# Kernel optimization log

Hardware: AMD Instinct MI355X
Metric: run time of the kernel (lower is better)

Reference implementation:

```python
import jax, jax.numpy as jnp
import numpy as np

KS = 3
STRIDE = 1
PAD = 1


def conv2d(x, w, b=None, stride=1, pad=0):
    out = jax.lax.conv_general_dilated(
        x, w, (stride, stride), [(pad, pad), (pad, pad)],
        dimension_numbers=('NCHW', 'OIHW', 'NCHW'))
    if b is not None:
        out = out + b[None, :, None, None]
    return out


def _get_p(offset, ks, stride):
    # offset: (b, 2N, h, w); returns sampling coords p = p_0 + p_n + offset
    b, c2, h, w = offset.shape
    N = c2 // 2
    r = (ks - 1) // 2
    pn_x, pn_y = jnp.meshgrid(jnp.arange(-r, r + 1), jnp.arange(-r, r + 1), indexing='ij')
    p_n = jnp.concatenate([pn_x.reshape(-1), pn_y.reshape(-1)]).astype(offset.dtype)  # (2N,)
    p0_x, p0_y = jnp.meshgrid(jnp.arange(1, h * stride + 1, stride),
                              jnp.arange(1, w * stride + 1, stride), indexing='ij')
    p0 = jnp.concatenate([jnp.broadcast_to(p0_x, (N, h, w)),
                          jnp.broadcast_to(p0_y, (N, h, w))], 0).astype(offset.dtype)  # (2N,h,w)
    return offset + p_n[None, :, None, None] + p0[None]


def _gather_hw(src, qx, qy):
    # src: (b,c,H,W); qx,qy: (b,h,w,N) int -> (b,c,h,w,N)
    b, c, H, W = src.shape
    flat = src.reshape(b, c, H * W)
    idx = (qx * W + qy).reshape(b, -1)
    out = jax.vmap(lambda f, i: f[:, i])(flat, idx)  # (b,c,h*w*N)
    return out.reshape(b, c, qx.shape[1], qx.shape[2], qx.shape[3])


def _bilinear(src_pad, p, Hc, Wc, N):
    # p: (b,h,w,2N); clamp bounds (Hc,Wc) follow the torch code (may differ from src_pad dims)
    px, py = p[..., :N], p[..., N:]
    fx, fy = jnp.floor(px), jnp.floor(py)
    qlt_x = jnp.clip(fx, 0, Hc - 1).astype(jnp.int32)
    qlt_y = jnp.clip(fy, 0, Wc - 1).astype(jnp.int32)
    qrb_x = jnp.clip(fx + 1, 0, Hc - 1).astype(jnp.int32)
    qrb_y = jnp.clip(fy + 1, 0, Wc - 1).astype(jnp.int32)
    pxc = jnp.clip(px, 0, Hc - 1)
    pyc = jnp.clip(py, 0, Wc - 1)
    g_lt = (1 + (qlt_x - pxc)) * (1 + (qlt_y - pyc))
    g_rb = (1 - (qrb_x - pxc)) * (1 - (qrb_y - pyc))
    g_lb = (1 + (qlt_x - pxc)) * (1 - (qrb_y - pyc))
    g_rt = (1 - (qrb_x - pxc)) * (1 + (qlt_y - pyc))
    v_lt = _gather_hw(src_pad, qlt_x, qlt_y)
    v_rb = _gather_hw(src_pad, qrb_x, qrb_y)
    v_lb = _gather_hw(src_pad, qlt_x, qrb_y)
    v_rt = _gather_hw(src_pad, qrb_x, qlt_y)
    return (g_lt[:, None] * v_lt + g_rb[:, None] * v_rb
            + g_lb[:, None] * v_lb + g_rt[:, None] * v_rt)


def setup_inputs() -> dict:
    key = jax.random.key(0)
    k1, k2, k3, k4 = jax.random.split(key, 4)
    B, C, H, W = 2, 64, 128, 128
    OUTC, KSZ = 64, KS
    N = KSZ * KSZ
    x = jax.random.normal(k1, (B, C, H, W), dtype=jnp.float32)
    depth = jax.random.uniform(k2, (B, 1, H, W), dtype=jnp.float32)
    w_p = jax.random.normal(k3, (2 * N, C, 3, 3), dtype=jnp.float32) * 0.01
    b_p = jnp.zeros((2 * N,), dtype=jnp.float32)
    w_conv = jax.random.normal(k4, (OUTC, C, KSZ, KSZ), dtype=jnp.float32) * 0.05
    return {'x': x, 'depth': depth, 'w_p': w_p, 'b_p': b_p, 'w_conv': w_conv}


def reference(x, depth, w_p, b_p, w_conv):
    ks, stride, pad = KS, STRIDE, PAD
    N = ks * ks
    b, c, H, W = x.shape
    offset = conv2d(x, w_p, b_p, stride=stride, pad=1)  # (b, 2N, h, w)
    depth_pad = jnp.pad(depth, ((0, 0), (0, 0), (pad, pad), (pad, pad)))
    # pass 1: sample depth; torch clamps against UNPADDED x dims here (quirk preserved)
    p = jnp.transpose(_get_p(offset, ks, stride), (0, 2, 3, 1))  # (b,h,w,2N)
    depth_offset = _bilinear(depth_pad, p, H, W, N)  # (b,1,h,w,N)
    depth_diff = jnp.abs(depth[..., None] - depth_offset)  # (b,1,h,w,N)
    depth_weight = jnp.exp(-4.0 * depth_diff) + 0.25
    dw = jnp.concatenate([depth_weight, depth_weight], axis=-1)  # (b,1,h,w,2N)
    dw = jnp.transpose(dw, (0, 4, 2, 3, 1))[..., 0]  # (b,2N,h,w)
    offset = offset * dw
    # pass 2: sample x from padded x, clamped to padded dims
    x_pad = jnp.pad(x, ((0, 0), (0, 0), (pad, pad), (pad, pad)))
    Hp, Wp = x_pad.shape[2], x_pad.shape[3]
    p = jnp.transpose(_get_p(offset, ks, stride), (0, 2, 3, 1))
    x_offset = _bilinear(x_pad, p, Hp, Wp, N)  # (b,c,h,w,N)
    m = jnp.exp(-1.0 * depth_diff)  # (b,1,h,w,N), broadcasts over c
    x_offset = x_offset * m
    # reshape (b,c,h,w,N) -> (b,c,h*ks,w*ks) matching _reshape_x_offset
    b2, c2, h, w, _ = x_offset.shape
    xo = x_offset.reshape(b2, c2, h, w, ks, ks)
    xo = jnp.transpose(xo, (0, 1, 2, 4, 3, 5)).reshape(b2, c2, h * ks, w * ks)
    out = conv2d(xo, w_conv, None, stride=ks, pad=0)  # (b,outc,h,w)
    return out
```

## Files before the change

kernel.cpp:

```cpp
#include <hip/hip_runtime.h>
#include <math.h>


typedef __attribute__((ext_vector_type(8))) short bf16x8;
typedef __attribute__((ext_vector_type(4))) short s16x4;
typedef __attribute__((ext_vector_type(4))) float f32x4;

#define MFMA16(a, b, c) __builtin_amdgcn_mfma_f32_16x16x32_bf16((a), (b), (c), 0, 0, 0)

__device__ __forceinline__ float bf2f(short v) {
    return __uint_as_float(((unsigned)(unsigned short)v) << 16);
}
__device__ __forceinline__ short f2bf(float f) {
    unsigned u = __float_as_uint(f);
    u = u + 0x7fffu + ((u >> 16) & 1u);
    return (short)(u >> 16);
}

__global__ __launch_bounds__(256) void k_prep(const float* __restrict__ x,
                                              const float* __restrict__ w_conv,
                                              const float* __restrict__ w_p,
                                              short* __restrict__ xT,
                                              short* __restrict__ xTlo,
                                              short* __restrict__ wK,
                                              short* __restrict__ wPh,
                                              short* __restrict__ wPl) {
    __shared__ short sH[128][72];
    __shared__ short sL[128][72];
    int bid = blockIdx.x;
    int tid = threadIdx.x;
    if (bid < 256) {
        int p = tid & 127;
        int halfc = tid >> 7;
        int pix0 = bid << 7;
        int b = pix0 >> 14;
        const float* xb = x + (size_t)b * 64 * 16384 + (pix0 & 16383);
#pragma unroll
        for (int cc = 0; cc < 8; ++cc) {
            int c0 = cc * 8 + halfc * 4;
            union { short s[4]; s16x4 v; } hi, lo;
#pragma unroll
            for (int e = 0; e < 4; ++e) {
                float v = xb[(c0 + e) * 16384 + p];
                short hb = f2bf(v);
                hi.s[e] = hb;
                lo.s[e] = f2bf(v - bf2f(hb));
            }
            *reinterpret_cast<s16x4*>(&sH[p][c0]) = hi.v;
            *reinterpret_cast<s16x4*>(&sL[p][c0]) = lo.v;
        }
        __syncthreads();
        short* xTo = xT   + ((size_t)pix0 << 6);
        short* xLo = xTlo + ((size_t)pix0 << 6);
#pragma unroll
        for (int r = 0; r < 4; ++r) {
            int u = (r << 8) + tid;
            int pp = u >> 3, ch8 = u & 7;
            *reinterpret_cast<bf16x8*>(xTo + pp * 64 + ch8 * 8) =
                *reinterpret_cast<const bf16x8*>(&sH[pp][ch8 * 8]);
            *reinterpret_cast<bf16x8*>(xLo + pp * 64 + ch8 * 8) =
                *reinterpret_cast<const bf16x8*>(&sL[pp][ch8 * 8]);
        }
    } else {
        int idx = (bid - 256) * 256 + tid;
        if (idx >= 55296) return;
        if (idx < 36864) {
            int e = idx & 7, o = (idx >> 3) & 63, h = (idx >> 9) & 3, s = idx >> 11;
            int k = s * 32 + h * 8 + e;
            int n = k >> 6, c = k & 63;
            wK[idx] = f2bf(w_conv[o * 576 + c * 9 + n]);
        } else {
            int j = idx - 36864;
            int e = j & 7, m = (j >> 3) & 31, h = (j >> 8) & 3, s = j >> 10;
            int k = s * 32 + h * 8 + e;
            int t = k >> 6, c = k & 63;
            float v = (m < 18) ? w_p[m * 576 + c * 9 + t] : 0.f;
            short hb = f2bf(v);
            wPh[j] = hb;
            wPl[j] = f2bf(v - bf2f(hb));
        }
    }
}

__global__ __launch_bounds__(256, 4) void k_fused(const short* __restrict__ xT,
                                                  const short* __restrict__ xTlo,
                                                  const short* __restrict__ wPh,
                                                  const short* __restrict__ wPl,
                                                  const short* __restrict__ wK,
                                                  const float* __restrict__ depth,
                                                  const float* __restrict__ b_p,
                                                  float* __restrict__ out) {
    __shared__ __align__(16) char smem[24880];
    short* win    = (short*)smem;
    float* part1  = (float*)(smem + 13440);
    float* dwin   = (float*)(smem + 18560);
    float* offs   = (float*)(smem + 18992);
    float* pmw    = (float*)(smem + 20272);
    float* accred = (float*)smem;
    float* obuf   = (float*)(smem + 13440);

    int tid = threadIdx.x;
    int lane = tid & 63;
    int wv = tid >> 6;
    int l15 = lane & 15, h = lane >> 4;
    int bid = blockIdx.x;
    int swz = (bid & 7) * 256 + (bid >> 3);
    int pb = swz << 4;
    int b = pb >> 14, i = (pb & 16383) >> 7, j0 = pb & 127;
    const short* xTb  = xT   + ((size_t)b << 20);
    const short* xTlb = xTlo + ((size_t)b << 20);
    const float* db = depth + (b << 14);

    for (int u = tid; u < 840; u += 256) {
        int c8 = u & 7, px = u >> 3;
        int wr = px / 21, wc = px % 21;
        int r = i - 2 + wr, c = j0 - 2 + wc;
        bf16x8 v = {0, 0, 0, 0, 0, 0, 0, 0};
        if ((unsigned)r < 128u && (unsigned)c < 128u)
            v = *reinterpret_cast<const bf16x8*>(xTb + ((size_t)(r * 128 + c) << 6) + c8 * 8);
        *reinterpret_cast<bf16x8*>((char*)win + px * 128 + ((c8 ^ (px & 7)) << 4)) = v;
    }
    if (tid < 105) {
        int wr = tid / 21, wc = tid % 21;
        int r = i - 2 + wr, c = j0 - 2 + wc;
        dwin[tid] = ((unsigned)r < 128u && (unsigned)c < 128u) ? db[r * 128 + c] : 0.f;
    }
    __syncthreads();

    f32x4 acc0 = {0.f, 0.f, 0.f, 0.f}, acc1 = {0.f, 0.f, 0.f, 0.f};
    for (int t = wv; t < 9; t += 4) {
        int wp = (t / 3 + 1) * 21 + (l15 + t % 3 + 1);
        int si = i + t / 3 - 1;
        int sj = j0 + l15 + t % 3 - 1;
        bool inb = ((unsigned)si < 128u && (unsigned)sj < 128u);
        size_t go = (size_t)(si * 128 + sj) << 6;
#pragma unroll
        for (int par = 0; par < 2; ++par) {
            int s_ = t * 2 + par;
            int c8 = par * 4 + h;
            bf16x8 bh = *reinterpret_cast<const bf16x8*>(
                (char*)win + wp * 128 + ((c8 ^ (wp & 7)) << 4));
            bf16x8 bl = {0, 0, 0, 0, 0, 0, 0, 0};
            if (inb) bl = *reinterpret_cast<const bf16x8*>(xTlb + go + c8 * 8);
            const short* wh_ = wPh + (size_t)((s_ * 4 + h) * 32 + l15) * 8;
            const short* wl_ = wPl + (size_t)((s_ * 4 + h) * 32 + l15) * 8;
            bf16x8 ah0 = *reinterpret_cast<const bf16x8*>(wh_);
            bf16x8 ah1 = *reinterpret_cast<const bf16x8*>(wh_ + 128);
            bf16x8 al0 = *reinterpret_cast<const bf16x8*>(wl_);
            bf16x8 al1 = *reinterpret_cast<const bf16x8*>(wl_ + 128);
            acc0 = MFMA16(ah0, bh, acc0);
            acc1 = MFMA16(ah1, bh, acc1);
            acc0 = MFMA16(ah0, bl, acc0);
            acc1 = MFMA16(ah1, bl, acc1);
            acc0 = MFMA16(al0, bh, acc0);
            acc1 = MFMA16(al1, bh, acc1);
        }
    }
#pragma unroll
    for (int r = 0; r < 4; ++r) {
        part1[wv * 320 + l15 * 20 + h * 4 + r] = acc0[r];
        int o1 = 16 + h * 4 + r;
        if (o1 < 18) part1[wv * 320 + l15 * 20 + o1] = acc1[r];
    }
    __syncthreads();
    if (tid < 128) {
        for (int u = tid; u < 288; u += 128) {
            int p = u / 18, o = u % 18;
            offs[p * 20 + o] = part1[p * 20 + o] + part1[320 + p * 20 + o] +
                               part1[640 + p * 20 + o] + part1[960 + p * 20 + o] + b_p[o];
        }
    }
    __syncthreads();

    int g = (wv << 2) + h;
    if (g < 9) {
        int n = g;
        float offx = offs[l15 * 20 + n];
        float offy = offs[l15 * 20 + 9 + n];
        float gx = (float)(n / 3 - 1 + i + 1);
        float gy = (float)(n % 3 - 1 + j0 + l15 + 1);
        float dctr = dwin[2 * 21 + l15 + 2];
        float p1x = offx + gx, p1y = offy + gy;
        float fx = floorf(p1x), fy = floorf(p1y);
        float qltx = fminf(fmaxf(fx, 0.f), 127.f);
        float qlty = fminf(fmaxf(fy, 0.f), 127.f);
        float qrbx = fminf(fmaxf(fx + 1.f, 0.f), 127.f);
        float qrby = fminf(fmaxf(fy + 1.f, 0.f), 127.f);
        float pxc = fminf(fmaxf(p1x, 0.f), 127.f);
        float pyc = fminf(fmaxf(p1y, 0.f), 127.f);
        float glt = (1.f + (qltx - pxc)) * (1.f + (qlty - pyc));
        float grb = (1.f - (qrbx - pxc)) * (1.f - (qrby - pyc));
        float glb = (1.f + (qltx - pxc)) * (1.f - (qrby - pyc));
        float grt = (1.f - (qrbx - pxc)) * (1.f + (qlty - pyc));
        int ilx = (int)qltx, ily = (int)qlty, irx = (int)qrbx, iry = (int)qrby;
        auto dv = [&](int qx, int qy) -> float {
            if (qx < 1 || qx > 128 || qy < 1 || qy > 128) return 0.f;
            int r = qx - 1, c = qy - 1;
            int wr = r - (i - 2), wc = c - (j0 - 2);
            if ((unsigned)wr < 5u && (unsigned)wc < 21u) return dwin[wr * 21 + wc];
            return db[r * 128 + c];
        };
        float dof = glt * dv(ilx, ily) + grb * dv(irx, iry) + glb * dv(ilx, iry) + grt * dv(irx, ily);
        float dd = fabsf(dctr - dof);
        float dwn = expf(-4.f * dd) + 0.25f;
        float mn = expf(-dd);
        float px = offx * dwn + gx;
        float py = offy * dwn + gy;
        float fx2 = floorf(px), fy2 = floorf(py);
        float xltx = fminf(fmaxf(fx2, 0.f), 129.f);
        float xlty = fminf(fmaxf(fy2, 0.f), 129.f);
        float xrbx = fminf(fmaxf(fx2 + 1.f, 0.f), 129.f);
        float xrby = fminf(fmaxf(fy2 + 1.f, 0.f), 129.f);
        float xpxc = fminf(fmaxf(px, 0.f), 129.f);
        float xpyc = fminf(fmaxf(py, 0.f), 129.f);
        float wlt = (1.f + (xltx - xpxc)) * (1.f + (xlty - xpyc));
        float wrb = (1.f - (xrbx - xpxc)) * (1.f - (xrby - xpyc));
        float wlb = (1.f + (xltx - xpxc)) * (1.f - (xrby - xpyc));
        float wrt = (1.f - (xrbx - xpxc)) * (1.f + (xlty - xpyc));
        int jlx = (int)xltx, jly = (int)xlty, jrx = (int)xrbx, jry = (int)xrby;
        float* d = pmw + (l15 * 9 + n) * 8;
        int* di = (int*)(d + 4);
        auto mk = [&](int qx, int qy, float gw, int slot) {
            bool ok = (qx >= 1 && qx <= 128 && qy >= 1 && qy <= 128);
            d[slot] = ok ? gw * mn : 0.f;
            int idx = 0;
            if (ok) {
                int r = qx - 1, c = qy - 1;
                int wr = r - (i - 2), wc = c - (j0 - 2);
                idx = ((unsigned)wr < 5u && (unsigned)wc < 21u) ? (wr * 21 + wc)
                                                                : (-1 - (r * 128 + c));
            }
            di[slot] = idx;
        };
        mk(jlx, jly, wlt, 0);
        mk(jrx, jry, wrb, 1);
        mk(jlx, jry, wlb, 2);
        mk(jrx, jly, wrt, 3);
    }
    __syncthreads();

    f32x4 A0 = {0.f, 0.f, 0.f, 0.f}, A1 = {0.f, 0.f, 0.f, 0.f};
    f32x4 A2 = {0.f, 0.f, 0.f, 0.f}, A3 = {0.f, 0.f, 0.f, 0.f};
    for (int n = wv; n < 9; n += 4) {
        const float* ww = pmw + (l15 * 9 + n) * 8;
        float4 w4 = *reinterpret_cast<const float4*>(ww);
        int4 i4 = *reinterpret_cast<const int4*>(ww + 4);
        const short* wk0 = wK + (size_t)((n * 8 + h) * 64 + l15) * 8;
        const short* wk1 = wk0 + 2048;
        bf16x8 a00 = *reinterpret_cast<const bf16x8*>(wk0);
        bf16x8 a01 = *reinterpret_cast<const bf16x8*>(wk0 + 128);
        bf16x8 a02 = *reinterpret_cast<const bf16x8*>(wk0 + 256);
        bf16x8 a03 = *reinterpret_cast<const bf16x8*>(wk0 + 384);
        bf16x8 a10 = *reinterpret_cast<const bf16x8*>(wk1);
        bf16x8 a11 = *reinterpret_cast<const bf16x8*>(wk1 + 128);
        bf16x8 a12 = *reinterpret_cast<const bf16x8*>(wk1 + 256);
        bf16x8 a13 = *reinterpret_cast<const bf16x8*>(wk1 + 384);
        const int* ip = &i4.x;
        const float* wp = &w4.x;
#pragma unroll
        for (int t = 0; t < 4; ++t) {
            int idx = ip[t];
            float w = wp[t];
            bf16x8 th0, th1;
            if (idx >= 0) {
                const char* base = (char*)win + idx * 128;
                th0 = *reinterpret_cast<const bf16x8*>(base + ((h ^ (idx & 7)) << 4));
                th1 = *reinterpret_cast<const bf16x8*>(base + (((4 + h) ^ (idx & 7)) << 4));
            } else {
                int gp = -1 - idx;
                const short* gb = xTb + ((size_t)gp << 6) + h * 8;
                th0 = *reinterpret_cast<const bf16x8*>(gb);
                th1 = *reinterpret_cast<const bf16x8*>(gb + 32);
            }
            f32x4 Z = {0.f, 0.f, 0.f, 0.f};
            f32x4 D0 = MFMA16(a00, th0, Z);
            f32x4 D1 = MFMA16(a01, th0, Z);
            f32x4 D2 = MFMA16(a02, th0, Z);
            f32x4 D3 = MFMA16(a03, th0, Z);
            D0 = MFMA16(a10, th1, D0);
            D1 = MFMA16(a11, th1, D1);
            D2 = MFMA16(a12, th1, D2);
            D3 = MFMA16(a13, th1, D3);
            A0 += w * D0;
            A1 += w * D1;
            A2 += w * D2;
            A3 += w * D3;
        }
    }
    __syncthreads();
    if (wv != 0) {
        float* ar = accred + (wv - 1) * 1024 + lane * 16;
        *reinterpret_cast<f32x4*>(ar)      = A0;
        *reinterpret_cast<f32x4*>(ar + 4)  = A1;
        *reinterpret_cast<f32x4*>(ar + 8)  = A2;
        *reinterpret_cast<f32x4*>(ar + 12) = A3;
    }
    __syncthreads();
    if (wv == 0) {
        const float* a1 = accred + lane * 16;
        const float* a2 = accred + 1024 + lane * 16;
        const float* a3 = accred + 2048 + lane * 16;
#pragma unroll
        for (int r = 0; r < 4; ++r) {
            obuf[(h * 4 + r) * 17 + l15]      = A0[r] + a1[r] + a2[r] + a3[r];
            obuf[(16 + h * 4 + r) * 17 + l15] = A1[r] + a1[4 + r] + a2[4 + r] + a3[4 + r];
            obuf[(32 + h * 4 + r) * 17 + l15] = A2[r] + a1[8 + r] + a2[8 + r] + a3[8 + r];
            obuf[(48 + h * 4 + r) * 17 + l15] = A3[r] + a1[12 + r] + a2[12 + r] + a3[12 + r];
        }
    }
    __syncthreads();
#pragma unroll
    for (int r = 0; r < 4; ++r) {
        int u = (r << 8) + tid;
        int o = u >> 4, p = u & 15;
        out[((size_t)(b * 64 + o) << 14) + (i << 7) + j0 + p] = obuf[o * 17 + p];
    }
}

extern "C" void kernel_launch(void* const* d_in, const int* in_sizes, int n_in,
                              void* d_out, int out_size, void* d_ws, size_t ws_size,
                              hipStream_t stream) {
    (void)in_sizes; (void)n_in; (void)out_size; (void)ws_size;
    const float* x      = (const float*)d_in[0];
    const float* depth  = (const float*)d_in[1];
    const float* w_p    = (const float*)d_in[2];
    const float* b_p    = (const float*)d_in[3];
    const float* w_conv = (const float*)d_in[4];
    float* out = (float*)d_out;

    char* wsb = (char*)d_ws;
    short* xT   = (short*)wsb;
    short* xTlo = (short*)(wsb + 4194304);
    short* wK   = (short*)(wsb + 8388608);
    short* wPh  = (short*)(wsb + 8462336);
    short* wPl  = (short*)(wsb + 8499200);

    hipLaunchKernelGGL(k_prep,  dim3(472),  dim3(256), 0, stream,
                       x, w_conv, w_p, xT, xTlo, wK, wPh, wPl);
    hipLaunchKernelGGL(k_fused, dim3(2048), dim3(256), 0, stream,
                       xT, xTlo, wPh, wPl, wK, depth, b_p, out);
}
```

Before: 42.41 us.

## Enlarge fused block tile to 64 pixels with 512 threads

Each block of the fused deformable-conv kernel now covers 64 pixels of a row instead of 16, using 512 threads (8 waves). Waves are split into 4 pixel groups times 2 channel halves, replacing the previous 4-way split over kernel taps. The larger shared input window (5x69 instead of 5x21) lowers the halo overhead and the number of redundant window loads per pixel. In exchange, LDS per block grows to about 79 KB and there are 512 blocks instead of 2048, which lowers occupancy and gives fewer blocks per CU.

```diff
diff --git a/kernel.cpp b/kernel.cpp
--- a/kernel.cpp
+++ b/kernel.cpp
@@ -82,7 +82,7 @@
     }
 }
 
-__global__ __launch_bounds__(256, 4) void k_fused(const short* __restrict__ xT,
+__global__ __launch_bounds__(512, 4) void k_fused(const short* __restrict__ xT,
                                                   const short* __restrict__ xTlo,
                                                   const short* __restrict__ wPh,
                                                   const short* __restrict__ wPl,
@@ -90,96 +90,98 @@
                                                   const float* __restrict__ depth,
                                                   const float* __restrict__ b_p,
                                                   float* __restrict__ out) {
-    __shared__ __align__(16) char smem[24880];
+    __shared__ __align__(16) char smem[79360];
     short* win    = (short*)smem;
-    float* part1  = (float*)(smem + 13440);
-    float* dwin   = (float*)(smem + 18560);
-    float* offs   = (float*)(smem + 18992);
-    float* pmw    = (float*)(smem + 20272);
+    float* dwin   = (float*)(smem + 44160);
+    float* part1  = (float*)(smem + 45568);
+    float* offs   = (float*)(smem + 55808);
+    float* pmw    = (float*)(smem + 60928);
     float* accred = (float*)smem;
-    float* obuf   = (float*)(smem + 13440);
+    float* obuf   = (float*)(smem + 16384);
 
     int tid = threadIdx.x;
     int lane = tid & 63;
     int wv = tid >> 6;
     int l15 = lane & 15, h = lane >> 4;
+    int ps = wv & 3;
+    int kh = wv >> 2;
+    int p0 = ps << 4;
     int bid = blockIdx.x;
-    int swz = (bid & 7) * 256 + (bid >> 3);
-    int pb = swz << 4;
+    int swz = (bid & 7) * 64 + (bid >> 3);
+    int pb = swz << 6;
     int b = pb >> 14, i = (pb & 16383) >> 7, j0 = pb & 127;
     const short* xTb  = xT   + ((size_t)b << 20);
     const short* xTlb = xTlo + ((size_t)b << 20);
     const float* db = depth + (b << 14);
 
-    for (int u = tid; u < 840; u += 256) {
+    for (int u = tid; u < 2760; u += 512) {
         int c8 = u & 7, px = u >> 3;
-        int wr = px / 21, wc = px % 21;
+        int wr = px / 69, wc = px % 69;
         int r = i - 2 + wr, c = j0 - 2 + wc;
         bf16x8 v = {0, 0, 0, 0, 0, 0, 0, 0};
         if ((unsigned)r < 128u && (unsigned)c < 128u)
             v = *reinterpret_cast<const bf16x8*>(xTb + ((size_t)(r * 128 + c) << 6) + c8 * 8);
         *reinterpret_cast<bf16x8*>((char*)win + px * 128 + ((c8 ^ (px & 7)) << 4)) = v;
     }
-    if (tid < 105) {
-        int wr = tid / 21, wc = tid % 21;
+    for (int u = tid; u < 345; u += 512) {
+        int wr = u / 69, wc = u % 69;
         int r = i - 2 + wr, c = j0 - 2 + wc;
-        dwin[tid] = ((unsigned)r < 128u && (unsigned)c < 128u) ? db[r * 128 + c] : 0.f;
+        dwin[u] = ((unsigned)r < 128u && (unsigned)c < 128u) ? db[r * 128 + c] : 0.f;
     }
     __syncthreads();
 
     f32x4 acc0 = {0.f, 0.f, 0.f, 0.f}, acc1 = {0.f, 0.f, 0.f, 0.f};
-    for (int t = wv; t < 9; t += 4) {
-        int wp = (t / 3 + 1) * 21 + (l15 + t % 3 + 1);
+    int c8p = kh * 4 + h;
+#pragma unroll
+    for (int t = 0; t < 9; ++t) {
+        int s_ = t * 2 + kh;
+        int wp = (t / 3 + 1) * 69 + (p0 + l15 + t % 3 + 1);
+        bf16x8 bh = *reinterpret_cast<const bf16x8*>(
+            (char*)win + wp * 128 + ((c8p ^ (wp & 7)) << 4));
         int si = i + t / 3 - 1;
-        int sj = j0 + l15 + t % 3 - 1;
-        bool inb = ((unsigned)si < 128u && (unsigned)sj < 128u);
-        size_t go = (size_t)(si * 128 + sj) << 6;
-#pragma unroll
-        for (int par = 0; par < 2; ++par) {
-            int s_ = t * 2 + par;
-            int c8 = par * 4 + h;
-            bf16x8 bh = *reinterpret_cast<const bf16x8*>(
-                (char*)win + wp * 128 + ((c8 ^ (wp & 7)) << 4));
-            bf16x8 bl = {0, 0, 0, 0, 0, 0, 0, 0};
-            if (inb) bl = *reinterpret_cast<const bf16x8*>(xTlb + go + c8 * 8);
-            const short* wh_ = wPh + (size_t)((s_ * 4 + h) * 32 + l15) * 8;
-            const short* wl_ = wPl + (size_t)((s_ * 4 + h) * 32 + l15) * 8;
-            bf16x8 ah0 = *reinterpret_cast<const bf16x8*>(wh_);
-            bf16x8 ah1 = *reinterpret_cast<const bf16x8*>(wh_ + 128);
-            bf16x8 al0 = *reinterpret_cast<const bf16x8*>(wl_);
-            bf16x8 al1 = *reinterpret_cast<const bf16x8*>(wl_ + 128);
-            acc0 = MFMA16(ah0, bh, acc0);
-            acc1 = MFMA16(ah1, bh, acc1);
-            acc0 = MFMA16(ah0, bl, acc0);
-            acc1 = MFMA16(ah1, bl, acc1);
-            acc0 = MFMA16(al0, bh, acc0);
-            acc1 = MFMA16(al1, bh, acc1);
-        }
-    }
-#pragma unroll
-    for (int r = 0; r < 4; ++r) {
-        part1[wv * 320 + l15 * 20 + h * 4 + r] = acc0[r];
-        int o1 = 16 + h * 4 + r;
-        if (o1 < 18) part1[wv * 320 + l15 * 20 + o1] = acc1[r];
-    }
-    __syncthreads();
-    if (tid < 128) {
-        for (int u = tid; u < 288; u += 128) {
-            int p = u / 18, o = u % 18;
-            offs[p * 20 + o] = part1[p * 20 + o] + part1[320 + p * 20 + o] +
-                               part1[640 + p * 20 + o] + part1[960 + p * 20 + o] + b_p[o];
-        }
-    }
-    __syncthreads();
-
-    int g = (wv << 2) + h;
-    if (g < 9) {
-        int n = g;
-        float offx = offs[l15 * 20 + n];
-        float offy = offs[l15 * 20 + 9 + n];
+        int sj = j0 + p0 + l15 + t % 3 - 1;
+        bf16x8 bl = {0, 0, 0, 0, 0, 0, 0, 0};
+        if ((unsigned)si < 128u && (unsigned)sj < 128u)
+            bl = *reinterpret_cast<const bf16x8*>(
+                xTlb + ((size_t)(si * 128 + sj) << 6) + c8p * 8);
+        const short* wh_ = wPh + (size_t)((s_ * 4 + h) * 32 + l15) * 8;
+        const short* wl_ = wPl + (size_t)((s_ * 4 + h) * 32 + l15) * 8;
+        bf16x8 ah0 = *reinterpret_cast<const bf16x8*>(wh_);
+        bf16x8 ah1 = *reinterpret_cast<const bf16x8*>(wh_ + 128);
+        bf16x8 al0 = *reinterpret_cast<const bf16x8*>(wl_);
+        bf16x8 al1 = *reinterpret_cast<const bf16x8*>(wl_ + 128);
+        acc0 = MFMA16(ah0, bh, acc0);
+        acc1 = MFMA16(ah1, bh, acc1);
+        acc0 = MFMA16(ah0, bl, acc0);
+        acc1 = MFMA16(ah1, bl, acc1);
+        acc0 = MFMA16(al0, bh, acc0);
+        acc1 = MFMA16(al1, bh, acc1);
+    }
+    {
+        float* pp = part1 + ((ps * 2 + kh) * 16 + l15) * 20;
+#pragma unroll
+        for (int r = 0; r < 4; ++r) {
+            pp[h * 4 + r] = acc0[r];
+            int o1 = 16 + h * 4 + r;
+            if (o1 < 18) pp[o1] = acc1[r];
+        }
+    }
+    __syncthreads();
+    for (int u = tid; u < 1152; u += 512) {
+        int p = u / 18, o = u % 18;
+        int pps = p >> 4, pl = p & 15;
+        offs[p * 20 + o] = part1[((pps * 2) * 16 + pl) * 20 + o] +
+                           part1[((pps * 2 + 1) * 16 + pl) * 20 + o] + b_p[o];
+    }
+    __syncthreads();
+
+    for (int u = tid; u < 576; u += 512) {
+        int p = u / 9, n = u % 9;
+        float offx = offs[p * 20 + n];
+        float offy = offs[p * 20 + 9 + n];
         float gx = (float)(n / 3 - 1 + i + 1);
-        float gy = (float)(n % 3 - 1 + j0 + l15 + 1);
-        float dctr = dwin[2 * 21 + l15 + 2];
+        float gy = (float)(n % 3 - 1 + j0 + p + 1);
+        float dctr = dwin[2 * 69 + p + 2];
         float p1x = offx + gx, p1y = offy + gy;
         float fx = floorf(p1x), fy = floorf(p1y);
         float qltx = fminf(fmaxf(fx, 0.f), 127.f);
@@ -197,7 +199,7 @@
             if (qx < 1 || qx > 128 || qy < 1 || qy > 128) return 0.f;
             int r = qx - 1, c = qy - 1;
             int wr = r - (i - 2), wc = c - (j0 - 2);
-            if ((unsigned)wr < 5u && (unsigned)wc < 21u) return dwin[wr * 21 + wc];
+            if ((unsigned)wr < 5u && (unsigned)wc < 69u) return dwin[wr * 69 + wc];
             return db[r * 128 + c];
         };
         float dof = glt * dv(ilx, ily) + grb * dv(irx, iry) + glb * dv(ilx, iry) + grt * dv(irx, ily);
@@ -218,7 +220,7 @@
         float wlb = (1.f + (xltx - xpxc)) * (1.f - (xrby - xpyc));
         float wrt = (1.f - (xrbx - xpxc)) * (1.f + (xlty - xpyc));
         int jlx = (int)xltx, jly = (int)xlty, jrx = (int)xrbx, jry = (int)xrby;
-        float* d = pmw + (l15 * 9 + n) * 8;
+        float* d = pmw + u * 8;
         int* di = (int*)(d + 4);
         auto mk = [&](int qx, int qy, float gw, int slot) {
             bool ok = (qx >= 1 && qx <= 128 && qy >= 1 && qy <= 128);
@@ -227,7 +229,7 @@
             if (ok) {
                 int r = qx - 1, c = qy - 1;
                 int wr = r - (i - 2), wc = c - (j0 - 2);
-                idx = ((unsigned)wr < 5u && (unsigned)wc < 21u) ? (wr * 21 + wc)
+                idx = ((unsigned)wr < 5u && (unsigned)wc < 69u) ? (wr * 69 + wc)
                                                                 : (-1 - (r * 128 + c));
             }
             di[slot] = idx;
@@ -241,8 +243,8 @@
 
     f32x4 A0 = {0.f, 0.f, 0.f, 0.f}, A1 = {0.f, 0.f, 0.f, 0.f};
     f32x4 A2 = {0.f, 0.f, 0.f, 0.f}, A3 = {0.f, 0.f, 0.f, 0.f};
-    for (int n = wv; n < 9; n += 4) {
-        const float* ww = pmw + (l15 * 9 + n) * 8;
+    for (int n = kh; n < 9; n += 2) {
+        const float* ww = pmw + (size_t)((p0 + l15) * 9 + n) * 8;
         float4 w4 = *reinterpret_cast<const float4*>(ww);
         int4 i4 = *reinterpret_cast<const int4*>(ww + 4);
         const short* wk0 = wK + (size_t)((n * 8 + h) * 64 + l15) * 8;
@@ -288,32 +290,31 @@
         }
     }
     __syncthreads();
-    if (wv != 0) {
-        float* ar = accred + (wv - 1) * 1024 + lane * 16;
+    if (kh == 1) {
+        float* ar = accred + (ps * 64 + lane) * 16;
         *reinterpret_cast<f32x4*>(ar)      = A0;
         *reinterpret_cast<f32x4*>(ar + 4)  = A1;
         *reinterpret_cast<f32x4*>(ar + 8)  = A2;
         *reinterpret_cast<f32x4*>(ar + 12) = A3;
     }
     __syncthreads();
-    if (wv == 0) {
-        const float* a1 = accred + lane * 16;
-        const float* a2 = accred + 1024 + lane * 16;
-        const float* a3 = accred + 2048 + lane * 16;
+    if (kh == 0) {
+        const float* ar = accred + (ps * 64 + lane) * 16;
+        int col = p0 + l15;
 #pragma unroll
         for (int r = 0; r < 4; ++r) {
-            obuf[(h * 4 + r) * 17 + l15]      = A0[r] + a1[r] + a2[r] + a3[r];
-            obuf[(16 + h * 4 + r) * 17 + l15] = A1[r] + a1[4 + r] + a2[4 + r] + a3[4 + r];
-            obuf[(32 + h * 4 + r) * 17 + l15] = A2[r] + a1[8 + r] + a2[8 + r] + a3[8 + r];
-            obuf[(48 + h * 4 + r) * 17 + l15] = A3[r] + a1[12 + r] + a2[12 + r] + a3[12 + r];
-        }
-    }
-    __syncthreads();
-#pragma unroll
-    for (int r = 0; r < 4; ++r) {
-        int u = (r << 8) + tid;
-        int o = u >> 4, p = u & 15;
-        out[((size_t)(b * 64 + o) << 14) + (i << 7) + j0 + p] = obuf[o * 17 + p];
+            obuf[(h * 4 + r) * 66 + col]      = A0[r] + ar[r];
+            obuf[(16 + h * 4 + r) * 66 + col] = A1[r] + ar[4 + r];
+            obuf[(32 + h * 4 + r) * 66 + col] = A2[r] + ar[8 + r];
+            obuf[(48 + h * 4 + r) * 66 + col] = A3[r] + ar[12 + r];
+        }
+    }
+    __syncthreads();
+#pragma unroll
+    for (int r = 0; r < 8; ++r) {
+        int u = (r << 9) + tid;
+        int o = u >> 6, p = u & 63;
+        out[((size_t)(b * 64 + o) << 14) + (i << 7) + j0 + p] = obuf[o * 66 + p];
     }
 }
 
@@ -335,8 +336,8 @@
     short* wPh  = (short*)(wsb + 8462336);
     short* wPl  = (short*)(wsb + 8499200);
 
-    hipLaunchKernelGGL(k_prep,  dim3(472),  dim3(256), 0, stream,
+    hipLaunchKernelGGL(k_prep,  dim3(472), dim3(256), 0, stream,
                        x, w_conv, w_p, xT, xTlo, wK, wPh, wPl);
-    hipLaunchKernelGGL(k_fused, dim3(2048), dim3(256), 0, stream,
+    hipLaunchKernelGGL(k_fused, dim3(512), dim3(512), 0, stream,
                        xT, xTlo, wPh, wPl, wK, depth, b_p, out);
 }
```

Measured after the change: 37.39 us. -11.8%, faster.
